# Kernel tuning notes

Hardware: AMD Instinct MI355X
Metric: run time of the kernel (lower is better)

The kernel has to match this reference:

```python
import jax, jax.numpy as jnp
import numpy as np

B, T, D, H, TW = 4, 2048, 2048, 8, 4
DH = D // H


def setup_inputs() -> dict:
    key = jax.random.key(0)
    ks = jax.random.split(key, 16)
    s = lambda k, shape, std: jax.random.normal(k, shape, dtype=jnp.float32) * std
    inp = {
        "x": jax.random.normal(ks[0], (B, T, D), dtype=jnp.float32),
        "segment_pos": jnp.tile(jnp.arange(T, dtype=jnp.int32), (B, 1)),
        # linear_y / linear_x: width -> lru_width, std = 1/sqrt(width)
        "Wy": s(ks[1], (D, D), (1.0 / D) ** 0.5),
        "by": jnp.zeros((D,), jnp.float32),
        "Wx": s(ks[2], (D, D), (1.0 / D) ** 0.5),
        "bx": jnp.zeros((D,), jnp.float32),
        # depthwise causal conv: [temporal_width, lru_width]
        "conv_w": s(ks[3], (TW, D), (1.0 / TW) ** 0.5),
        "conv_b": jnp.zeros((D,), jnp.float32),
        # RG-LRU block-diagonal gates: [H, D/H, D/H]
        "gx_w": s(ks[4], (H, DH, DH), (1.0 / DH) ** 0.5),
        "gx_b": jnp.zeros((H, DH), jnp.float32),
        "ga_w": s(ks[5], (H, DH, DH), (1.0 / DH) ** 0.5),
        "ga_b": jnp.zeros((H, DH), jnp.float32),
        # a_param: softplus(a_param) > 0 controls decay rate
        "a_param": jnp.log(jnp.exp(jax.random.uniform(ks[6], (D,), minval=0.3, maxval=0.9)) - 1.0 + 1e-6),
        # linear_out: lru_width -> width, std = 1/sqrt(lru_width)
        "Wout": s(ks[7], (D, D), (1.0 / D) ** 0.5),
        "bout": jnp.zeros((D,), jnp.float32),
    }
    return inp


def _causal_conv1d(x, w, b, segment_pos):
    # depthwise causal conv over time; contributions from other segments masked
    t = x.shape[1]
    acc = jnp.zeros_like(x)
    for i in range(TW):
        shift = TW - 1 - i  # input at t - shift, weighted by w[i]
        xs = x if shift == 0 else jnp.pad(x, ((0, 0), (shift, 0), (0, 0)))[:, :t]
        mask = (segment_pos >= shift)[..., None].astype(x.dtype)
        acc = acc + xs * mask * w[i]
    return acc + b


def _rg_lru(x, segment_pos, gx_w, gx_b, ga_w, ga_b, a_param):
    b, t, d = x.shape
    xr = x.reshape(b, t, H, DH)
    gate_x = jax.nn.sigmoid(jnp.einsum("bthi,hij->bthj", xr, gx_w) + gx_b).reshape(b, t, d)
    gate_a = jax.nn.sigmoid(jnp.einsum("bthi,hij->bthj", xr, ga_w) + ga_b).reshape(b, t, d)
    log_a = -8.0 * gate_a * jax.nn.softplus(a_param)  # [B,T,D]
    a = jnp.exp(log_a)
    reset = (segment_pos == 0)[..., None]  # [B,T,1]
    multiplier = jnp.sqrt(jnp.maximum(1.0 - jnp.exp(2.0 * log_a), 0.0))
    multiplier = jnp.where(reset, 1.0, multiplier)
    normed = x * gate_x * multiplier
    a_scan = jnp.where(reset, 0.0, a)

    def step(h, inputs):
        a_t, x_t = inputs
        h = a_t * h + x_t
        return h, h

    h0 = jnp.zeros((b, d), x.dtype)
    _, ys = jax.lax.scan(step, h0, (a_scan.transpose(1, 0, 2), normed.transpose(1, 0, 2)))
    return ys.transpose(1, 0, 2)


def reference(x, segment_pos, Wy, by, Wx, bx, conv_w, conv_b, gx_w, gx_b, ga_w, ga_b, a_param, Wout, bout):
    y = jax.nn.gelu(x @ Wy.T + by, approximate=True)
    x_proj = x @ Wx.T + bx
    x_conv = _causal_conv1d(x_proj, conv_w, conv_b, segment_pos)
    x_lru = _rg_lru(x_conv, segment_pos, gx_w, gx_b, ga_w, ga_b, a_param)
    out = (x_lru * y) @ Wout.T + bout
    return out
```

## Files before the change

kernel.cpp:

```cpp
#include <hip/hip_runtime.h>
#include <cstdint>
#include <cstddef>

typedef __bf16 bf16;
typedef __bf16 bf16x8 __attribute__((ext_vector_type(8)));
typedef float f32x4 __attribute__((ext_vector_type(4)));

#define BDIM 4
#define TDIM 2048
#define DDIM 2048
#define HDIM 8
#define DHD 256
#define MTOT 8192
#define NCHUNK 64
#define LCHUNK 32

__device__ __forceinline__ void stage16(const bf16* g, bf16* l) {
  __builtin_amdgcn_global_load_lds(
      (const __attribute__((address_space(1))) void*)g,
      (__attribute__((address_space(3))) void*)l, 16, 0, 0);
}

#define BARX() __builtin_amdgcn_s_barrier()
#define SCHB() __builtin_amdgcn_sched_barrier(0)
#define WAITVM(N) asm volatile("s_waitcnt vmcnt(" #N ")")

__device__ __forceinline__ float sigmoid_f(float x) {
  return __fdividef(1.f, 1.f + __expf(-x));
}
__device__ __forceinline__ float gelu_tanh(float v) {
  float u = 0.7978845608028654f * (v + 0.044715f * v * v * v);
  u = fminf(fmaxf(u, -15.f), 15.f);
  float t = __expf(2.f * u);
  return 0.5f * v * (1.f + __fdividef(t - 1.f, t + 1.f));
}
__device__ __forceinline__ float softplus_f(float x) {
  return __logf(1.f + __expf(x));
}

__global__ __launch_bounds__(256) void f2b(const float* __restrict__ src,
                                           bf16* __restrict__ dst) {
  size_t i = ((size_t)blockIdx.x * 256 + threadIdx.x) * 8;
  const float4 a = *(const float4*)(src + i);
  const float4 b = *(const float4*)(src + i + 4);
  bf16x8 r;
  r[0] = (bf16)a.x; r[1] = (bf16)a.y; r[2] = (bf16)a.z; r[3] = (bf16)a.w;
  r[4] = (bf16)b.x; r[5] = (bf16)b.y; r[6] = (bf16)b.z; r[7] = (bf16)b.w;
  *(bf16x8*)(dst + i) = r;
}

template <typename TO, int EPI>
__global__ __launch_bounds__(512, 2) void gemm256(
    const bf16* __restrict__ A, const bf16* __restrict__ Bm,
    const float* __restrict__ bias, TO* __restrict__ C,
    int K, int lda, int ldb, int ldc) {
  const int gx = gridDim.x, gy = gridDim.y;
  const int nwg = gx * gy;
  const int did = blockIdx.x + gx * blockIdx.y;
  const int cpx = nwg >> 3;
  const int lid = (did & 7) * cpx + (did >> 3);
  const int n0 = (lid % gx) * 256;
  const int m0 = (lid / gx) * 256;

  __shared__ bf16 sA0[256 * 64];
  __shared__ bf16 sA1[256 * 64];
  __shared__ bf16 sB0[256 * 64];
  __shared__ bf16 sB1[256 * 64];
  const int tid = threadIdx.x;
  const int lane = tid & 63;
  const int wid = tid >> 6;
  const int wr = wid >> 2;
  const int wc = wid & 3;
  const int quad = lane >> 4;
  const int l15 = lane & 15;

  const int sr = tid >> 3;
  const int ks8 = ((tid & 7) ^ (sr & 7)) << 3;
  const bf16* Ag = A + (size_t)(m0 + sr) * lda + ks8;
  const bf16* Bg = Bm + (size_t)(n0 + sr) * ldb + ks8;

  const int swz0 = ((quad) ^ (l15 & 7)) << 3;
  const int swz1 = ((4 + quad) ^ (l15 & 7)) << 3;

  f32x4 acc[8][4];
#pragma unroll
  for (int i = 0; i < 8; ++i)
#pragma unroll
    for (int j = 0; j < 4; ++j)
#pragma unroll
      for (int r = 0; r < 4; ++r) acc[i][j][r] = 0.f;

  const int NT = K >> 6;

#define STG_A(ARR, H, TK)                                                     \
  do {                                                                        \
    _Pragma("unroll") for (int j_ = 0; j_ < 2; ++j_) {                        \
      const int c_ = (H) * 2 + j_;                                            \
      stage16(Ag + (size_t)(c_ * 64) * lda + (size_t)(TK) * 64,               \
              &ARR[(c_ * 64 + wid * 8) * 64]);                                \
    }                                                                         \
  } while (0)
#define STG_B(ARR, H, TK)                                                     \
  do {                                                                        \
    _Pragma("unroll") for (int j_ = 0; j_ < 2; ++j_) {                        \
      const int c_ = (H) * 2 + j_;                                            \
      stage16(Bg + (size_t)(c_ * 64) * ldb + (size_t)(TK) * 64,               \
              &ARR[(c_ * 64 + wid * 8) * 64]);                                \
    }                                                                         \
  } while (0)

  bf16x8 aq0[4][2], aq1[4][2], b0[2][2], b1[2][2];

#define RDA(DST, MH, ARR)                                                     \
  do {                                                                        \
    _Pragma("unroll") for (int mi_ = 0; mi_ < 4; ++mi_) {                     \
      const int arow_ = wr * 128 + (MH) * 64 + mi_ * 16 + l15;                \
      DST[mi_][0] = *(const bf16x8*)(&ARR[arow_ * 64] + swz0);                \
      DST[mi_][1] = *(const bf16x8*)(&ARR[arow_ * 64] + swz1);                \
    }                                                                         \
  } while (0)
#define RDB(DST, NH, ARR)                                                     \
  do {                                                                        \
    _Pragma("unroll") for (int ni_ = 0; ni_ < 2; ++ni_) {                     \
      const int brow_ = wc * 64 + (NH) * 32 + ni_ * 16 + l15;                 \
      DST[ni_][0] = *(const bf16x8*)(&ARR[brow_ * 64] + swz0);                \
      DST[ni_][1] = *(const bf16x8*)(&ARR[brow_ * 64] + swz1);                \
    }                                                                         \
  } while (0)
#define MFMAQ(MH, NH, AA, BB)                                                 \
  do {                                                                        \
    __builtin_amdgcn_s_setprio(1);                                            \
    _Pragma("unroll") for (int mi_ = 0; mi_ < 4; ++mi_)                       \
        _Pragma("unroll") for (int ni_ = 0; ni_ < 2; ++ni_) {                 \
      acc[(MH)*4 + mi_][(NH)*2 + ni_] = __builtin_amdgcn_mfma_f32_16x16x32_bf16( \
          AA[mi_][0], BB[ni_][0], acc[(MH)*4 + mi_][(NH)*2 + ni_], 0, 0, 0);  \
      acc[(MH)*4 + mi_][(NH)*2 + ni_] = __builtin_amdgcn_mfma_f32_16x16x32_bf16( \
          AA[mi_][1], BB[ni_][1], acc[(MH)*4 + mi_][(NH)*2 + ni_], 0, 0, 0);  \
    }                                                                         \
    __builtin_amdgcn_s_setprio(0);                                            \
  } while (0)

#define TILE(SAs, SBs, SAo, SBo, T)                                           \
  do {                                                                        \
    const int tn_ = ((T) + 1 < NT) ? (T) + 1 : NT - 1;                        \
    const int tnn_ = ((T) + 2 < NT) ? (T) + 2 : NT - 1;                       \
                                                                     \
    WAITVM(4);                                                                \
    SCHB();                                                                   \
    STG_B(SBo, 1, tn_);                                                       \
    RDB(b1, 1, SBs);                                                          \
    MFMAQ(0, 0, aq0, b0);                                                     \
    BARX();                                                                   \
                                                                     \
    STG_A(SAo, 1, tn_);                                                       \
    RDA(aq1, 1, SAs);                                                         \
    MFMAQ(0, 1, aq0, b1);                                                     \
    BARX();                                                                   \
                                                                     \
    STG_B(SBs, 0, tnn_);                                                      \
    MFMAQ(1, 0, aq1, b0);                                                     \
    BARX();                                                                   \
                                                                     \
    WAITVM(6);                                                                \
    SCHB();                                                                   \
    STG_A(SAs, 0, tnn_);                                                      \
    RDA(aq0, 0, SAo);                                                         \
    RDB(b0, 0, SBo);                                                          \
    MFMAQ(1, 1, aq1, b1);                                                     \
    BARX();                                                                   \
  } while (0)

  STG_B(sB0, 0, 0); STG_A(sA0, 0, 0);
  STG_B(sB0, 1, 0); STG_A(sA0, 1, 0);
  STG_B(sB1, 0, 1); STG_A(sA1, 0, 1);
  WAITVM(8);
  SCHB();
  BARX();
  RDA(aq0, 0, sA0);
  RDB(b0, 0, sB0);

  for (int t = 0; t < NT; t += 2) {
    TILE(sA0, sB0, sA1, sB1, t);
    TILE(sA1, sB1, sA0, sB0, t + 1);
  }
  WAITVM(0);

#undef STG_A
#undef STG_B
#undef RDA
#undef RDB
#undef MFMAQ
#undef TILE

  float bv[4];
#pragma unroll
  for (int nn = 0; nn < 4; ++nn) bv[nn] = bias[n0 + wc * 64 + nn * 16 + l15];
#pragma unroll
  for (int mm = 0; mm < 8; ++mm) {
#pragma unroll
    for (int r = 0; r < 4; ++r) {
      const int m = m0 + wr * 128 + mm * 16 + quad * 4 + r;
      TO* Crow = C + (size_t)m * ldc + n0 + wc * 64 + l15;
#pragma unroll
      for (int nn = 0; nn < 4; ++nn) {
        float v = acc[mm][nn][r] + bv[nn];
        if (EPI == 1) v = gelu_tanh(v);
        Crow[nn * 16] = (TO)v;
      }
    }
  }
}

__global__ __launch_bounds__(256) void gate_gemm(
    const bf16* __restrict__ xconv,
    const bf16* __restrict__ gxT, const bf16* __restrict__ gaT,
    bf16* __restrict__ gxr, bf16* __restrict__ gar) {
  const int h = blockIdx.z >> 1;
  const int g = blockIdx.z & 1;
  const bf16* A = xconv + h * DHD;
  const bf16* Bm = (g ? gaT : gxT) + (size_t)h * DHD * DHD;
  bf16* C = (g ? gar : gxr) + h * DHD;
  const int n0 = blockIdx.x * 128;
  const int m0 = blockIdx.y * 128;
  __shared__ bf16 As[128 * 32];
  __shared__ bf16 Bs[128 * 32];
  const int tid = threadIdx.x;
  const int lane = tid & 63;
  const int wid = tid >> 6;
  const int waveM = wid >> 1, waveN = wid & 1;
  const int quad = lane >> 4;
  const int l15 = lane & 15;
  const int srow = lane >> 2;
  const int scol = (lane & 3) * 8;

  f32x4 acc[4][4];
#pragma unroll
  for (int i = 0; i < 4; ++i)
#pragma unroll
    for (int j = 0; j < 4; ++j)
#pragma unroll
      for (int r = 0; r < 4; ++r) acc[i][j][r] = 0.f;

  for (int k0 = 0; k0 < DHD; k0 += 32) {
    if (k0) __syncthreads();
#pragma unroll
    for (int cc = 0; cc < 2; ++cc) {
      const int q = wid * 2 + cc;
      const int row = q * 16 + srow;
      stage16(A + (size_t)(m0 + row) * DDIM + k0 + scol, As + q * 512);
      stage16(Bm + (size_t)(n0 + row) * DHD + k0 + scol, Bs + q * 512);
    }
    __syncthreads();
    bf16x8 af[4], bfr[4];
#pragma unroll
    for (int i = 0; i < 4; ++i) {
      af[i]  = *(const bf16x8*)&As[(waveM * 64 + i * 16 + l15) * 32 + quad * 8];
      bfr[i] = *(const bf16x8*)&Bs[(waveN * 64 + i * 16 + l15) * 32 + quad * 8];
    }
#pragma unroll
    for (int i = 0; i < 4; ++i)
#pragma unroll
      for (int j = 0; j < 4; ++j)
        acc[i][j] = __builtin_amdgcn_mfma_f32_16x16x32_bf16(af[i], bfr[j], acc[i][j], 0, 0, 0);
  }

#pragma unroll
  for (int j = 0; j < 4; ++j) {
    const int n = n0 + waveN * 64 + j * 16 + l15;
#pragma unroll
    for (int i = 0; i < 4; ++i) {
#pragma unroll
      for (int r = 0; r < 4; ++r) {
        const int m = m0 + waveM * 64 + i * 16 + quad * 4 + r;
        C[(size_t)m * DDIM + n] = (bf16)acc[i][j][r];
      }
    }
  }
}

__global__ __launch_bounds__(256) void conv_kernel(
    const bf16* __restrict__ xp, const float* __restrict__ cw,
    const float* __restrict__ cb, const int* __restrict__ segp,
    bf16* __restrict__ xc) {
  int v = blockIdx.x * 256 + threadIdx.x;
  int dv = v & (DDIM / 8 - 1);
  int m = v >> 8;
  int d0 = dv * 8;
  int t = m & (TDIM - 1);
  int sp = segp[m];
  float acc[8];
#pragma unroll
  for (int j = 0; j < 8; ++j) acc[j] = cb[d0 + j];
#pragma unroll
  for (int i = 0; i < 4; ++i) {
    int shift = 3 - i;
    if (t >= shift && sp >= shift) {
      bf16x8 xv = *(const bf16x8*)&xp[(size_t)(m - shift) * DDIM + d0];
#pragma unroll
      for (int j = 0; j < 8; ++j) acc[j] = fmaf((float)xv[j], cw[i * DDIM + d0 + j], acc[j]);
    }
  }
  bf16x8 o;
#pragma unroll
  for (int j = 0; j < 8; ++j) o[j] = (bf16)acc[j];
  *(bf16x8*)&xc[(size_t)m * DDIM + d0] = o;
}

__global__ __launch_bounds__(256) void transpose_gates(
    const float* __restrict__ gxw, const float* __restrict__ gaw,
    bf16* __restrict__ gxT, bf16* __restrict__ gaT) {
  __shared__ bf16 tile[32][33];
  int zz = blockIdx.z;
  int h = zz >> 1;
  const float* src = (zz & 1) ? gaw : gxw;
  bf16* dst = (zz & 1) ? gaT : gxT;
  int j0 = blockIdx.x * 32;
  int i0 = blockIdx.y * 32;
  int r = threadIdx.x >> 5;
  int c = threadIdx.x & 31;
  for (int rr = r; rr < 32; rr += 8)
    tile[rr][c] = (bf16)src[(size_t)(h * DHD + i0 + rr) * DHD + j0 + c];
  __syncthreads();
  for (int rr = r; rr < 32; rr += 8)
    dst[(size_t)(h * DHD + j0 + rr) * DHD + i0 + c] = tile[c][rr];
}

__device__ __forceinline__ void lru_elem(float pgx, float pga, float xc,
                                         float spv, bool reset,
                                         float& a, float& nr) {
  const float gx = sigmoid_f(pgx);
  const float ga = sigmoid_f(pga);
  const float la = -8.f * ga * spv;
  a = reset ? 0.f : __expf(la);
  const float mult = reset ? 1.f : sqrtf(fmaxf(1.f - __expf(2.f * la), 0.f));
  nr = xc * gx * mult;
}

__global__ __launch_bounds__(256) void scan_phase1(
    const bf16* __restrict__ gxr, const bf16* __restrict__ gar,
    const bf16* __restrict__ xconv,
    const float* __restrict__ gxb, const float* __restrict__ gab,
    const float* __restrict__ apar, const int* __restrict__ segp,
    float* __restrict__ chA, float* __restrict__ chH) {
  int idx = blockIdx.x * 256 + threadIdx.x;
  int d = idx & (DDIM - 1);
  int c = (idx >> 11) & (NCHUNK - 1);
  int b = idx >> 17;
  const float gxbv = gxb[d], gabv = gab[d];
  const float spv = softplus_f(apar[d]);
  const int mrow = b * TDIM + c * LCHUNK;
  size_t base = (size_t)mrow * DDIM + d;
  float A = 1.f, hh = 0.f;
  for (int i = 0; i < LCHUNK; ++i) {
    size_t o = base + (size_t)i * DDIM;
    float a, nr;
    lru_elem((float)gxr[o] + gxbv, (float)gar[o] + gabv, (float)xconv[o],
             spv, segp[mrow + i] == 0, a, nr);
    hh = fmaf(a, hh, nr);
    A *= a;
  }
  int ci = (b * NCHUNK + c) * DDIM + d;
  chA[ci] = A;
  chH[ci] = hh;
}

__global__ __launch_bounds__(256) void scan_phase2(
    const float* __restrict__ chA, const float* __restrict__ chH,
    float* __restrict__ hst) {
  int idx = blockIdx.x * 256 + threadIdx.x;
  int d = idx & (DDIM - 1);
  int b = idx >> 11;
  float s = 0.f;
  for (int c = 0; c < NCHUNK; ++c) {
    int ci = (b * NCHUNK + c) * DDIM + d;
    hst[ci] = s;
    s = fmaf(chA[ci], s, chH[ci]);
  }
}

__global__ __launch_bounds__(256) void scan_phase3(
    const bf16* __restrict__ gxr, const bf16* __restrict__ gar,
    const bf16* __restrict__ xconv,
    const float* __restrict__ gxb, const float* __restrict__ gab,
    const float* __restrict__ apar, const int* __restrict__ segp,
    const float* __restrict__ hst, bf16* __restrict__ yz) {
  int idx = blockIdx.x * 256 + threadIdx.x;
  int d = idx & (DDIM - 1);
  int c = (idx >> 11) & (NCHUNK - 1);
  int b = idx >> 17;
  const float gxbv = gxb[d], gabv = gab[d];
  const float spv = softplus_f(apar[d]);
  const int mrow = b * TDIM + c * LCHUNK;
  size_t base = (size_t)mrow * DDIM + d;
  float hh = hst[(b * NCHUNK + c) * DDIM + d];
  for (int i = 0; i < LCHUNK; ++i) {
    size_t o = base + (size_t)i * DDIM;
    float a, nr;
    lru_elem((float)gxr[o] + gxbv, (float)gar[o] + gabv, (float)xconv[o],
             spv, segp[mrow + i] == 0, a, nr);
    hh = fmaf(a, hh, nr);
    yz[o] = (bf16)(hh * (float)yz[o]);
  }
}

extern "C" void kernel_launch(void* const* d_in, const int* in_sizes, int n_in,
                              void* d_out, int out_size, void* d_ws, size_t ws_size,
                              hipStream_t stream) {
  const float* x    = (const float*)d_in[0];
  const int*   segp = (const int*)d_in[1];
  const float* Wy   = (const float*)d_in[2];
  const float* by   = (const float*)d_in[3];
  const float* Wx   = (const float*)d_in[4];
  const float* bx   = (const float*)d_in[5];
  const float* cw   = (const float*)d_in[6];
  const float* cb   = (const float*)d_in[7];
  const float* gxw  = (const float*)d_in[8];
  const float* gxb  = (const float*)d_in[9];
  const float* gaw  = (const float*)d_in[10];
  const float* gab  = (const float*)d_in[11];
  const float* apar = (const float*)d_in[12];
  const float* Wout = (const float*)d_in[13];
  const float* bout = (const float*)d_in[14];

  const size_t MD = (size_t)MTOT * DDIM;
  const size_t WD = (size_t)DDIM * DDIM;
  bf16* xb    = (bf16*)d_out;
  bf16* xproj = (bf16*)((char*)d_out + MD * 2);
  bf16* xconv = xb;
  bf16* gxr   = xproj;

  char* ws = (char*)d_ws;
  bf16*  gar = (bf16*)ws;
  bf16*  W1  = (bf16*)(ws + MD * 2);
  bf16*  WB1 = (bf16*)(ws + 2 * MD * 2);
  bf16*  WB2 = (bf16*)(ws + 2 * MD * 2 + WD * 2);
  char*  tail = ws + 2 * MD * 2 + 2 * WD * 2;
  const size_t GW = (size_t)HDIM * DHD * DHD * 2;
  const size_t CH = (size_t)BDIM * NCHUNK * DDIM * 4;
  bf16*  gxT = (bf16*)tail;
  bf16*  gaT = (bf16*)(tail + GW);
  float* chA = (float*)(tail + 2 * GW);
  float* chH = (float*)(tail + 2 * GW + CH);
  float* hst = (float*)(tail + 2 * GW + 2 * CH);

  dim3 blk(256);
  f2b<<<dim3(MD / 2048), blk, 0, stream>>>(x, xb);
  f2b<<<dim3(WD / 2048), blk, 0, stream>>>(Wx, WB1);
  f2b<<<dim3(WD / 2048), blk, 0, stream>>>(Wy, WB2);
  transpose_gates<<<dim3(8, 8, 16), blk, 0, stream>>>(gxw, gaw, gxT, gaT);

  gemm256<bf16, 0><<<dim3(8, 32), dim3(512), 0, stream>>>(xb, WB1, bx, xproj, DDIM, DDIM, DDIM, DDIM);
  gemm256<bf16, 1><<<dim3(8, 32), dim3(512), 0, stream>>>(xb, WB2, by, W1, DDIM, DDIM, DDIM, DDIM);

  conv_kernel<<<dim3(MTOT * (DDIM / 8) / 256), blk, 0, stream>>>(xproj, cw, cb, segp, xconv);

  gate_gemm<<<dim3(2, 64, 16), blk, 0, stream>>>(xconv, gxT, gaT, gxr, gar);

  scan_phase1<<<dim3(BDIM * NCHUNK * DDIM / 256), blk, 0, stream>>>(
      gxr, gar, xconv, gxb, gab, apar, segp, chA, chH);
  scan_phase2<<<dim3(BDIM * DDIM / 256), blk, 0, stream>>>(chA, chH, hst);
  scan_phase3<<<dim3(BDIM * NCHUNK * DDIM / 256), blk, 0, stream>>>(
      gxr, gar, xconv, gxb, gab, apar, segp, hst, W1);

  f2b<<<dim3(WD / 2048), blk, 0, stream>>>(Wout, WB1);
  gemm256<float, 0><<<dim3(8, 32), dim3(512), 0, stream>>>(W1, WB1, bout, (float*)d_out, DDIM, DDIM, DDIM, DDIM);
}
```

Before: 410.2 us.

## Restructure GEMM main loop to single A-fragment buffer with explicit LDS waits

Reworks the ping-pong GEMM tile schedule so A fragments are held in one register set instead of two. LDS reads are now issued at the start of each quarter-step and guarded by explicit lgkmcnt waits, and the global->LDS staging order and vmcnt waits are reordered. The intent is lower register pressure and a tighter read/stage/MFMA interleave. The cost is that LDS reads are no longer prefetched a full MFMA block ahead, which can expose LDS latency, and the extra barriers add synchronisation.

```diff
diff --git a/kernel.cpp b/kernel.cpp
--- a/kernel.cpp
+++ b/kernel.cpp
@@ -24,6 +24,7 @@
 #define BARX() __builtin_amdgcn_s_barrier()
 #define SCHB() __builtin_amdgcn_sched_barrier(0)
 #define WAITVM(N) asm volatile("s_waitcnt vmcnt(" #N ")")
+#define WAITLG(N) asm volatile("s_waitcnt lgkmcnt(" #N ")")
 
 __device__ __forceinline__ float sigmoid_f(float x) {
   return __fdividef(1.f, 1.f + __expf(-x));
@@ -109,14 +110,14 @@
     }                                                                         \
   } while (0)
 
-  bf16x8 aq0[4][2], aq1[4][2], b0[2][2], b1[2][2];
-
-#define RDA(DST, MH, ARR)                                                     \
+  bf16x8 af[4][2], b0[2][2], b1[2][2];
+
+#define RDA(MH, ARR)                                                          \
   do {                                                                        \
     _Pragma("unroll") for (int mi_ = 0; mi_ < 4; ++mi_) {                     \
       const int arow_ = wr * 128 + (MH) * 64 + mi_ * 16 + l15;                \
-      DST[mi_][0] = *(const bf16x8*)(&ARR[arow_ * 64] + swz0);                \
-      DST[mi_][1] = *(const bf16x8*)(&ARR[arow_ * 64] + swz1);                \
+      af[mi_][0] = *(const bf16x8*)(&ARR[arow_ * 64] + swz0);                 \
+      af[mi_][1] = *(const bf16x8*)(&ARR[arow_ * 64] + swz1);                 \
     }                                                                         \
   } while (0)
 #define RDB(DST, NH, ARR)                                                     \
@@ -127,15 +128,15 @@
       DST[ni_][1] = *(const bf16x8*)(&ARR[brow_ * 64] + swz1);                \
     }                                                                         \
   } while (0)
-#define MFMAQ(MH, NH, AA, BB)                                                 \
+#define MFMAQ(MH, NH, BB)                                                     \
   do {                                                                        \
     __builtin_amdgcn_s_setprio(1);                                            \
     _Pragma("unroll") for (int mi_ = 0; mi_ < 4; ++mi_)                       \
         _Pragma("unroll") for (int ni_ = 0; ni_ < 2; ++ni_) {                 \
       acc[(MH)*4 + mi_][(NH)*2 + ni_] = __builtin_amdgcn_mfma_f32_16x16x32_bf16( \
-          AA[mi_][0], BB[ni_][0], acc[(MH)*4 + mi_][(NH)*2 + ni_], 0, 0, 0);  \
+          af[mi_][0], BB[ni_][0], acc[(MH)*4 + mi_][(NH)*2 + ni_], 0, 0, 0);  \
       acc[(MH)*4 + mi_][(NH)*2 + ni_] = __builtin_amdgcn_mfma_f32_16x16x32_bf16( \
-          AA[mi_][1], BB[ni_][1], acc[(MH)*4 + mi_][(NH)*2 + ni_], 0, 0, 0);  \
+          af[mi_][1], BB[ni_][1], acc[(MH)*4 + mi_][(NH)*2 + ni_], 0, 0, 0);  \
     }                                                                         \
     __builtin_amdgcn_s_setprio(0);                                            \
   } while (0)
@@ -144,40 +145,47 @@
   do {                                                                        \
     const int tn_ = ((T) + 1 < NT) ? (T) + 1 : NT - 1;                        \
     const int tnn_ = ((T) + 2 < NT) ? (T) + 2 : NT - 1;                       \
-                                                                     \
+                                                           \
+    RDA(0, SAs);                                                              \
+    RDB(b0, 0, SBs);                                                          \
+    STG_A(SAo, 1, tn_);                                                       \
+    WAITLG(8);                                                                \
+    BARX();                                                                   \
+    WAITLG(0);                                                                \
+    SCHB();                                                                   \
+    MFMAQ(0, 0, b0);                                                          \
+    BARX();                                                                   \
+                                                            \
+    RDB(b1, 1, SBs);                                                          \
+    STG_B(SBo, 1, tn_);                                                       \
+    BARX();                                                                   \
+    WAITLG(0);                                                                \
+    SCHB();                                                                   \
+    MFMAQ(0, 1, b1);                                                          \
+    BARX();                                                                   \
+                                                 \
+    RDA(1, SAs);                                                              \
+    STG_B(SBs, 0, tnn_);                                                      \
+    BARX();                                                                   \
+    WAITLG(0);                                                                \
+    SCHB();                                                                   \
+    MFMAQ(1, 0, b0);                                                          \
+    BARX();                                                                   \
+                                  \
+    STG_A(SAs, 0, tnn_);                                                      \
+    BARX();                                                                   \
+    SCHB();                                                                   \
+    MFMAQ(1, 1, b1);                                                          \
     WAITVM(4);                                                                \
-    SCHB();                                                                   \
-    STG_B(SBo, 1, tn_);                                                       \
-    RDB(b1, 1, SBs);                                                          \
-    MFMAQ(0, 0, aq0, b0);                                                     \
-    BARX();                                                                   \
-                                                                     \
-    STG_A(SAo, 1, tn_);                                                       \
-    RDA(aq1, 1, SAs);                                                         \
-    MFMAQ(0, 1, aq0, b1);                                                     \
-    BARX();                                                                   \
-                                                                     \
-    STG_B(SBs, 0, tnn_);                                                      \
-    MFMAQ(1, 0, aq1, b0);                                                     \
-    BARX();                                                                   \
-                                                                     \
-    WAITVM(6);                                                                \
-    SCHB();                                                                   \
-    STG_A(SAs, 0, tnn_);                                                      \
-    RDA(aq0, 0, SAo);                                                         \
-    RDB(b0, 0, SBo);                                                          \
-    MFMAQ(1, 1, aq1, b1);                                                     \
     BARX();                                                                   \
   } while (0)
 
   STG_B(sB0, 0, 0); STG_A(sA0, 0, 0);
-  STG_B(sB0, 1, 0); STG_A(sA0, 1, 0);
+  STG_A(sA0, 1, 0); STG_B(sB0, 1, 0);
   STG_B(sB1, 0, 1); STG_A(sA1, 0, 1);
-  WAITVM(8);
+  WAITVM(4);
   SCHB();
   BARX();
-  RDA(aq0, 0, sA0);
-  RDB(b0, 0, sB0);
 
   for (int t = 0; t < NT; t += 2) {
     TILE(sA0, sB0, sA1, sB1, t);
```

Result: slower. 435.3 us (+6.1%).
